# Kernel optimization log

Hardware: AMD Instinct MI355X
Metric: run time of the kernel (lower is better)

The kernel has to match this reference:

```python
import jax, jax.numpy as jnp
import numpy as np

D_MODEL = 128; D_STATE = 16; D_CONV = 4; EXPAND = 2
D_INNER = EXPAND * D_MODEL          # 256
DT_RANK = (D_MODEL + 15) // 16      # 8 (ceil(d_model/16), Mamba default)
B, NF, H, W = 4, 32, 16, 16         # L = NF*H*W = 8192 tokens


def _layer_norm(x, w, b, eps=1e-5):
    m = x.mean(-1, keepdims=True)
    v = ((x - m) ** 2).mean(-1, keepdims=True)
    return (x - m) * jax.lax.rsqrt(v + eps) * w + b


def _causal_conv(x, w, b):
    # x: [B, L, D_INNER]; w: [D_INNER, 1, D_CONV] depthwise causal conv along L
    y = jax.lax.conv_general_dilated(
        jnp.swapaxes(x, 1, 2), w, (1,), [(D_CONV - 1, 0)],
        dimension_numbers=('NCH', 'OIH', 'NCH'), feature_group_count=D_INNER)
    return jnp.swapaxes(y + b[None, :, None], 1, 2)


def _mamba_dir(xi, z, conv_w, conv_b, xproj_w, dtproj_w, dtproj_b, A_log, Dskip):
    # One direction of the bidirectional Mamba block (selective scan).
    xc = jax.nn.silu(_causal_conv(xi, conv_w, conv_b))            # [B,L,Di]
    dbl = xc @ xproj_w.T                                          # [B,L,dt_rank+2n]
    dt_r, Bm, Cm = jnp.split(dbl, [DT_RANK, DT_RANK + D_STATE], axis=-1)
    dt = jax.nn.softplus(dt_r @ dtproj_w.T + dtproj_b)            # [B,L,Di]
    A = -jnp.exp(A_log)                                           # [Di,n]

    def step(h, inp):
        dt_t, B_t, C_t, x_t = inp                                 # [B,Di],[B,n],[B,n],[B,Di]
        h = jnp.exp(dt_t[:, :, None] * A) * h + (dt_t * x_t)[:, :, None] * B_t[:, None, :]
        return h, jnp.einsum('bdn,bn->bd', h, C_t)

    h0 = jnp.zeros((xi.shape[0], D_INNER, D_STATE), xi.dtype)
    xs = tuple(jnp.swapaxes(a, 0, 1) for a in (dt, Bm, Cm, xc))   # L-leading
    _, ys = jax.lax.scan(step, h0, xs)                            # [L,B,Di]
    y = jnp.swapaxes(ys, 0, 1) + xc * Dskip
    return y * jax.nn.silu(z)


def setup_inputs() -> dict:
    key = jax.random.key(0)
    ks = jax.random.split(key, 12)
    wrand = lambda k, shape: jax.random.normal(k, shape, jnp.float32) * 0.02
    # S4D-real init: A = [1..d_state] per channel
    A_init = jnp.log(jnp.tile(jnp.arange(1, D_STATE + 1, dtype=jnp.float32)[None, :], (D_INNER, 1)))
    dt_bias = jnp.full((D_INNER,), -4.6, jnp.float32)  # softplus^-1(~0.01)
    return {
        'x': jax.random.normal(ks[0], (B, D_MODEL, NF, H, W), jnp.float32),
        'ln1_w': jnp.ones((D_MODEL,), jnp.float32), 'ln1_b': jnp.zeros((D_MODEL,), jnp.float32),
        'ln2_w': jnp.ones((D_MODEL,), jnp.float32), 'ln2_b': jnp.zeros((D_MODEL,), jnp.float32),
        'in_proj_w': wrand(ks[1], (2 * D_INNER, D_MODEL)),
        'out_proj_w': wrand(ks[2], (D_MODEL, D_INNER)),
        'conv_w_f': wrand(ks[3], (D_INNER, 1, D_CONV)), 'conv_b_f': jnp.zeros((D_INNER,), jnp.float32),
        'xproj_w_f': wrand(ks[4], (DT_RANK + 2 * D_STATE, D_INNER)),
        'dtproj_w_f': wrand(ks[5], (D_INNER, DT_RANK)), 'dtproj_b_f': dt_bias,
        'A_log_f': A_init, 'D_f': jnp.ones((D_INNER,), jnp.float32),
        'conv_w_b': wrand(ks[6], (D_INNER, 1, D_CONV)), 'conv_b_b': jnp.zeros((D_INNER,), jnp.float32),
        'xproj_w_b': wrand(ks[7], (DT_RANK + 2 * D_STATE, D_INNER)),
        'dtproj_w_b': wrand(ks[8], (D_INNER, DT_RANK)), 'dtproj_b_b': dt_bias,
        'A_log_b': A_init, 'D_b': jnp.ones((D_INNER,), jnp.float32),
    }


def reference(x, ln1_w, ln1_b, ln2_w, ln2_b, in_proj_w, out_proj_w,
              conv_w_f, conv_b_f, xproj_w_f, dtproj_w_f, dtproj_b_f, A_log_f, D_f,
              conv_w_b, conv_b_b, xproj_w_b, dtproj_w_b, dtproj_b_b, A_log_b, D_b):
    b, d, nf, h, w = x.shape
    L = nf * h * w
    x_flat = jnp.swapaxes(x.reshape(b, d, L), 1, 2)               # [B,L,d_model]
    xn = _layer_norm(x_flat, ln1_w, ln1_b)
    xz = xn @ in_proj_w.T                                          # [B,L,2*Di]
    xi, z = jnp.split(xz, 2, axis=-1)
    y_f = _mamba_dir(xi, z, conv_w_f, conv_b_f, xproj_w_f, dtproj_w_f, dtproj_b_f, A_log_f, D_f)
    y_b = _mamba_dir(xi[:, ::-1], z[:, ::-1], conv_w_b, conv_b_b, xproj_w_b,
                     dtproj_w_b, dtproj_b_b, A_log_b, D_b)[:, ::-1]
    out = (y_f + y_b) @ out_proj_w.T                               # shared out_proj
    x_out = _layer_norm(x_flat + out, ln2_w, ln2_b)                # residual + norm2
    return jnp.swapaxes(x_out, 1, 2).reshape(b, d, nf, h, w)
```

## Files before the change

kernel.cpp:

```cpp
#include <hip/hip_runtime.h>

#define NB   4
#define LSEQ 8192
#define DM   128
#define DI   256
#define NS   16
#define RK   8
#define NCH  256
#define LC   32
#define MTOT (NB*LSEQ)
#define LOG2E 1.44269504088896340736f
#define LN2f  0.69314718055994530942f

#if __has_builtin(__builtin_amdgcn_exp2f)
__device__ __forceinline__ float fexp2(float x){ return __builtin_amdgcn_exp2f(x); }
#else
__device__ __forceinline__ float fexp2(float x){ return exp2f(x); }
#endif
#if __has_builtin(__builtin_amdgcn_logf)
__device__ __forceinline__ float flog2(float x){ return __builtin_amdgcn_logf(x); }
#else
__device__ __forceinline__ float flog2(float x){ return log2f(x); }
#endif
#if __has_builtin(__builtin_amdgcn_rcpf)
__device__ __forceinline__ float frcp(float x){ return __builtin_amdgcn_rcpf(x); }
#else
__device__ __forceinline__ float frcp(float x){ return 1.f/x; }
#endif
__device__ __forceinline__ float fexpn(float x){ return fexp2(x*LOG2E); }
__device__ __forceinline__ float fsilu(float x){ return x*frcp(1.f + fexpn(-x)); }
__device__ __forceinline__ float fsoftplus(float x){
  return fmaxf(x,0.f) + flog2(1.f + fexpn(-fabsf(x)))*LN2f;
}

__device__ __forceinline__ unsigned short f2bf(float v){
  unsigned int u = __float_as_uint(v);
  return (unsigned short)((u + 0x7FFFu + ((u >> 16) & 1u)) >> 16);
}
__device__ __forceinline__ float bf2f(unsigned short h){
  return __uint_as_float(((unsigned int)h) << 16);
}

typedef __attribute__((ext_vector_type(8))) short bf16x8;
typedef __attribute__((ext_vector_type(4))) float f32x4;

__global__ __launch_bounds__(256) void k_prep_w(
    const float* __restrict__ w, unsigned short* __restrict__ hi, unsigned short* __restrict__ lo,
    const float* __restrict__ xwf, const float* __restrict__ xwb, unsigned short* __restrict__ xwbf,
    const float* __restrict__ wop, unsigned short* __restrict__ wopbf)
{
  int i = blockIdx.x*256 + threadIdx.x;
  if (i < 65536) {
    float v = w[i];
    unsigned short h = f2bf(v);
    hi[i] = h;
    lo[i] = f2bf(v - bf2f(h));
  } else if (i < 90112) {
    int j = i - 65536;
    int dirw = j / 12288;
    int rem = j - dirw*12288;
    int row = rem >> 8, k = rem & 255;
    const float* src = dirw ? xwb : xwf;
    xwbf[j] = (row < 40) ? f2bf(src[row*256 + k]) : (unsigned short)0;
  } else {
    int j = i - 90112;
    wopbf[j] = f2bf(wop[j]);
  }
}

__global__ __launch_bounds__(256) void k_ln(
    const float* __restrict__ x, const float* __restrict__ ln1w, const float* __restrict__ ln1b,
    unsigned short* __restrict__ xnh, unsigned short* __restrict__ xnl)
{
  __shared__ float a_s[DM][65];
  __shared__ float mS[64], rS[64];
  const int tid = threadIdx.x;
  const int m0 = blockIdx.x * 64;
  const int b = m0 >> 13, l0 = m0 & (LSEQ-1);
  const float* xb = x + b*DM*LSEQ;
#pragma unroll
  for (int i = 0; i < 32; ++i) {
    int idx = tid + i*256;
    int d = idx >> 6, l = idx & 63;
    a_s[d][l] = xb[d*LSEQ + l0 + l];
  }
  __syncthreads();
  {
    int p = tid & 3, l = tid >> 2;
    float s = 0.f, q = 0.f;
#pragma unroll
    for (int jj = 0; jj < 32; ++jj) {
      float v = a_s[p + 4*jj][l];
      s += v; q += v*v;
    }
    s += __shfl_xor(s,1); s += __shfl_xor(s,2);
    q += __shfl_xor(q,1); q += __shfl_xor(q,2);
    float m = s*(1.f/DM);
    float var = q*(1.f/DM) - m*m;
    if (p == 0) { mS[l] = m; rS[l] = rsqrtf(var + 1e-5f); }
  }
  __syncthreads();
#pragma unroll
  for (int i = 0; i < 32; ++i) {
    int idx = tid + i*256;
    int l = idx >> 7, d = idx & 127;
    float v = (a_s[d][l] - mS[l])*rS[l]*ln1w[d] + ln1b[d];
    unsigned short h = f2bf(v);
    xnh[(m0+l)*DM + d] = h;
    xnl[(m0+l)*DM + d] = f2bf(v - bf2f(h));
  }
}

__global__ __launch_bounds__(256) void k_gemm_in(
    const unsigned short* __restrict__ xnh, const unsigned short* __restrict__ xnl,
    const unsigned short* __restrict__ wh,  const unsigned short* __restrict__ wl,
    float* __restrict__ xi, float* __restrict__ zz)
{
  __shared__ char lds[65536];
  const int tid = threadIdx.x;
  const int m0 = blockIdx.x * 64;
  const int n0 = blockIdx.y * 64;
  const unsigned short* srcs[4] = { xnh + m0*DM, xnl + m0*DM, wh + n0*DM, wl + n0*DM };
#pragma unroll
  for (int p = 0; p < 4; ++p) {
#pragma unroll
    for (int i = 0; i < 4; ++i) {
      int u = tid + i*256;
      int row = u >> 4, c = u & 15;
      int dstu = p*1024 + row*16 + (c ^ (row & 7));
      *(uint4*)(lds + dstu*16) = *(const uint4*)(srcs[p] + row*DM + c*8);
    }
  }
  __syncthreads();
  const int wid = tid >> 6, lane = tid & 63;
  const int m0w = (wid & 1)*32, n0w = (wid >> 1)*32;
  const int lr = lane & 15, kg = lane >> 4;
  bf16x8 ah[2][4], al[2][4], bh[2][4], bl[2][4];
#pragma unroll
  for (int mi = 0; mi < 2; ++mi) {
    int row = m0w + mi*16 + lr;
#pragma unroll
    for (int kk = 0; kk < 4; ++kk) {
      int slot = (kk*4 + kg) ^ (row & 7);
      ah[mi][kk] = *(const bf16x8*)(lds + 0     + row*256 + slot*16);
      al[mi][kk] = *(const bf16x8*)(lds + 16384 + row*256 + slot*16);
    }
  }
#pragma unroll
  for (int nj = 0; nj < 2; ++nj) {
    int row = n0w + nj*16 + lr;
#pragma unroll
    for (int kk = 0; kk < 4; ++kk) {
      int slot = (kk*4 + kg) ^ (row & 7);
      bh[nj][kk] = *(const bf16x8*)(lds + 32768 + row*256 + slot*16);
      bl[nj][kk] = *(const bf16x8*)(lds + 49152 + row*256 + slot*16);
    }
  }
  f32x4 acc[2][2];
#pragma unroll
  for (int mi = 0; mi < 2; ++mi)
#pragma unroll
    for (int nj = 0; nj < 2; ++nj) acc[mi][nj] = 0.f;
#pragma unroll
  for (int kk = 0; kk < 4; ++kk)
#pragma unroll
    for (int mi = 0; mi < 2; ++mi)
#pragma unroll
      for (int nj = 0; nj < 2; ++nj)
        acc[mi][nj] = __builtin_amdgcn_mfma_f32_16x16x32_bf16(ah[mi][kk], bh[nj][kk], acc[mi][nj], 0,0,0);
#pragma unroll
  for (int kk = 0; kk < 4; ++kk)
#pragma unroll
    for (int mi = 0; mi < 2; ++mi)
#pragma unroll
      for (int nj = 0; nj < 2; ++nj)
        acc[mi][nj] = __builtin_amdgcn_mfma_f32_16x16x32_bf16(ah[mi][kk], bl[nj][kk], acc[mi][nj], 0,0,0);
#pragma unroll
  for (int kk = 0; kk < 4; ++kk)
#pragma unroll
    for (int mi = 0; mi < 2; ++mi)
#pragma unroll
      for (int nj = 0; nj < 2; ++nj)
        acc[mi][nj] = __builtin_amdgcn_mfma_f32_16x16x32_bf16(al[mi][kk], bh[nj][kk], acc[mi][nj], 0,0,0);
  float* base = (n0 < 256) ? xi : zz;
  const int ncol0 = (n0 < 256) ? n0 : n0 - 256;
#pragma unroll
  for (int mi = 0; mi < 2; ++mi)
#pragma unroll
    for (int nj = 0; nj < 2; ++nj) {
      int n_g = ncol0 + n0w + nj*16 + lr;
#pragma unroll
      for (int r = 0; r < 4; ++r) {
        int m_g = m0 + m0w + mi*16 + kg*4 + r;
        base[m_g*DI + n_g] = acc[mi][nj][r];
      }
    }
}

__global__ __launch_bounds__(256) void k_conv_xproj(
  const float* __restrict__ xi,
  const float* __restrict__ cwf, const float* __restrict__ cbf,
  const float* __restrict__ cwb, const float* __restrict__ cbb,
  const unsigned short* __restrict__ xwbf,
  float* __restrict__ dtr, float* __restrict__ Bm, float* __restrict__ Cm)
{
  __shared__ char lds[57344];
  const int tid = threadIdx.x, bid = blockIdx.x;
  const int lt = bid & (LSEQ/64 - 1);
  const int b  = (bid >> 7) & 3;
  const int dir = bid >> 9;
  const int l0 = lt*64;
  const int db = dir*NB + b;
  const unsigned short* xwp = xwbf + dir*48*256;
#pragma unroll
  for (int i = 0; i < 6; ++i) {
    int u = tid + i*256;
    int row = u >> 5, s = u & 31;
    *(uint4*)(lds + 32768 + row*512 + ((s ^ (row & 7))<<4)) =
        *(const uint4*)(xwp + row*256 + s*8);
  }
  const float* cw  = dir ? cwb : cwf;
  const float* cbp = dir ? cbb : cbf;
  const int d = tid;
  const float w0 = cw[d*4+0], w1 = cw[d*4+1], w2 = cw[d*4+2], w3 = cw[d*4+3];
  const float bias = cbp[d];
  const int g0 = dir ? (LSEQ-1-l0) : l0;
  const int stp = dir ? -DI : DI;
  const float* xp = xi + (b*LSEQ)*DI + d + g0*DI;
  float h3 = 0.f, h2 = 0.f, h1 = 0.f;
  if (l0 >= 3) { h3 = xp[-3*stp]; h2 = xp[-2*stp]; h1 = xp[-1*stp]; }
  float r0 = xp[0], r1 = xp[stp], r2 = xp[2*stp], r3 = xp[3*stp];
  for (int j = 0; j < 64; j += 4) {
    float v0 = r0, v1 = r1, v2 = r2, v3 = r3;
    if (j + 4 < 64) {
      const float* q = xp + (j+4)*stp;
      r0 = q[0]; r1 = q[stp]; r2 = q[2*stp]; r3 = q[3*stp];
    }
    float a;
#pragma unroll
    for (int u = 0; u < 4; ++u) {
      float vv = (u==0)?v0:(u==1)?v1:(u==2)?v2:v3;
      a = bias + w0*h3 + w1*h2 + w2*h1 + w3*vv;
      int row = j + u;
      *(unsigned short*)(lds + row*512 + ((((d>>3) ^ (row&7))<<4) + ((d&7)<<1))) = f2bf(fsilu(a));
      h3 = h2; h2 = h1; h1 = vv;
    }
  }
  __syncthreads();
  const int wid = tid >> 6, lane = tid & 63;
  const int lr = lane & 15, kg = lane >> 4;
  const int arow = wid*16 + lr;
  f32x4 acc[3];
#pragma unroll
  for (int j = 0; j < 3; ++j) acc[j] = 0.f;
#pragma unroll
  for (int t = 0; t < 8; ++t) {
    bf16x8 af = *(const bf16x8*)(lds + arow*512 + (((t*4+kg) ^ (arow&7))<<4));
#pragma unroll
    for (int j = 0; j < 3; ++j) {
      int wrow = j*16 + lr;
      bf16x8 bfr = *(const bf16x8*)(lds + 32768 + wrow*512 + (((t*4+kg) ^ (wrow&7))<<4));
      acc[j] = __builtin_amdgcn_mfma_f32_16x16x32_bf16(af, bfr, acc[j], 0,0,0);
    }
  }
  const int base_l = (db*LSEQ + l0) + wid*16 + kg*4;
#pragma unroll
  for (int j = 0; j < 3; ++j) {
    int col = j*16 + lr;
#pragma unroll
    for (int r = 0; r < 4; ++r) {
      int gl = base_l + r;
      float v = acc[j][r];
      if (col < 8)       dtr[gl*RK + col] = v;
      else if (col < 24) Bm[gl*NS + col - 8] = v;
      else if (col < 40) Cm[gl*NS + col - 24] = v;
    }
  }
}

__global__ __launch_bounds__(256) void k_scan_local(
  const float* __restrict__ xi, const float* __restrict__ dtr, const float* __restrict__ Bm,
  const float* __restrict__ cwf, const float* __restrict__ cbf,
  const float* __restrict__ cwb, const float* __restrict__ cbb,
  const float* __restrict__ dtwf, const float* __restrict__ dtbf,
  const float* __restrict__ dtwb, const float* __restrict__ dtbb,
  const float* __restrict__ alogf, const float* __restrict__ alogb,
  float* __restrict__ hloc, float* __restrict__ sumdt)
{
  __shared__ float Bc[LC][NS];
  __shared__ float dts[LC][RK];
  const int tid = threadIdx.x, bid = blockIdx.x;
  const int c = bid & (NCH-1), b = (bid>>8)&3, dir = bid>>10;
  const int db = dir*NB + b;
  const int l0 = c*LC;
  for (int i = tid; i < LC*NS; i += 256) (&Bc[0][0])[i]  = Bm[(db*LSEQ + l0)*NS + i];
  for (int i = tid; i < LC*RK; i += 256) (&dts[0][0])[i] = dtr[(db*LSEQ + l0)*RK + i];
  const float* cw  = dir ? cwb : cwf;
  const float* cbp = dir ? cbb : cbf;
  const float* dtw = dir ? dtwb : dtwf;
  const float* dtbp= dir ? dtbb : dtbf;
  const float* alog= dir ? alogb : alogf;
  const int d = tid;
  const float w0 = cw[d*4+0], w1 = cw[d*4+1], w2 = cw[d*4+2], w3 = cw[d*4+3];
  const float cbias = cbp[d];
  float dw[RK];
#pragma unroll
  for (int r = 0; r < RK; ++r) dw[r] = dtw[d*RK+r];
  const float dtbv = dtbp[d];
  float A2[NS];
#pragma unroll
  for (int n = 0; n < NS; ++n) A2[n] = -fexpn(alog[d*NS+n]) * LOG2E;
  const float a20 = A2[0];
  bool pw = true;
#pragma unroll
  for (int n = 1; n < NS; ++n) pw = pw && (fabsf(A2[n] - (n+1)*a20) <= 1e-3f*fabsf(A2[n]));
  float h[NS];
#pragma unroll
  for (int n = 0; n < NS; ++n) h[n] = 0.f;
  const int g0 = dir ? (LSEQ-1-l0) : l0;
  const int stp = dir ? -DI : DI;
  const float* xp = xi + (b*LSEQ)*DI + d + g0*DI;
  float h3=0.f, h2=0.f, h1=0.f;
  if (l0 >= 3) { h3 = xp[-3*stp]; h2 = xp[-2*stp]; h1 = xp[-1*stp]; }
  float r0 = xp[0], r1 = xp[stp], r2 = xp[2*stp], r3 = xp[3*stp];
  __syncthreads();
  float sac = 0.f;
  for (int j = 0; j < LC; j += 4) {
    float v0=r0, v1=r1, v2=r2, v3=r3;
    if (j + 4 < LC) { const float* q = xp + (j+4)*stp; r0=q[0]; r1=q[stp]; r2=q[2*stp]; r3=q[3*stp]; }
#pragma unroll
    for (int u = 0; u < 4; ++u) {
      float v = (u==0)?v0:(u==1)?v1:(u==2)?v2:v3;
      float a = cbias + w0*h3 + w1*h2 + w2*h1 + w3*v;
      float xc = fsilu(a);
      float dd8[RK];
      *(float4*)(dd8+0) = *(const float4*)&dts[j+u][0];
      *(float4*)(dd8+4) = *(const float4*)&dts[j+u][4];
      float sd = dtbv;
#pragma unroll
      for (int r = 0; r < RK; ++r) sd = fmaf(dw[r], dd8[r], sd);
      float dt = fsoftplus(sd);
      sac += dt;
      float dx = dt*xc;
      float bb[NS];
      *(float4*)(bb+0)  = *(const float4*)&Bc[j+u][0];
      *(float4*)(bb+4)  = *(const float4*)&Bc[j+u][4];
      *(float4*)(bb+8)  = *(const float4*)&Bc[j+u][8];
      *(float4*)(bb+12) = *(const float4*)&Bc[j+u][12];
      float earr[NS];
      if (pw) {
        float e1 = fexp2(a20*dt);
        float e = e1; earr[0] = e;
#pragma unroll
        for (int n = 1; n < NS; ++n) { e *= e1; earr[n] = e; }
      } else {
#pragma unroll
        for (int n = 0; n < NS; ++n) earr[n] = fexp2(A2[n]*dt);
      }
#pragma unroll
      for (int n = 0; n < NS; ++n) h[n] = fmaf(h[n], earr[n], dx*bb[n]);
      h3 = h2; h2 = h1; h1 = v;
    }
  }
  const int hb = ((db*NCH + c)*DI + d)*NS;
#pragma unroll
  for (int n = 0; n < NS; ++n) hloc[hb+n] = h[n];
  sumdt[(db*NCH + c)*DI + d] = sac;
}

__global__ __launch_bounds__(64) void k_prefix(
  float* __restrict__ hloc, const float* __restrict__ sumdt,
  const float* __restrict__ alogf, const float* __restrict__ alogb)
{
  const int gid = blockIdx.x*64 + threadIdx.x;
  const int n = gid & 15;
  const int d = (gid >> 4) & 255;
  const int db = gid >> 12;
  const float* alog = (db >= NB) ? alogb : alogf;
  const float a2 = -fexpn(alog[d*NS+n]) * LOG2E;
  const int HS = DI*NS;
  float* hp = hloc + (size_t)db*NCH*HS + d*NS + n;
  const float* sp = sumdt + (size_t)db*NCH*DI + d;
  float hr = 0.f;
  float bl[16], bs[16];
#pragma unroll
  for (int j = 0; j < 16; ++j) { bl[j] = hp[j*HS]; bs[j] = sp[j*DI]; }
  for (int blk = 0; blk < NCH/16; ++blk) {
    float nl[16], nsv[16];
    if (blk < NCH/16 - 1) {
#pragma unroll
      for (int j = 0; j < 16; ++j) { nl[j] = hp[(blk*16+16+j)*HS]; nsv[j] = sp[(blk*16+16+j)*DI]; }
    }
#pragma unroll
    for (int j = 0; j < 16; ++j) {
      float hl = bl[j];
      hp[(blk*16+j)*HS] = hr;
      hr = fmaf(fexp2(a2*bs[j]), hr, hl);
    }
    if (blk < NCH/16 - 1) {
#pragma unroll
      for (int j = 0; j < 16; ++j) { bl[j] = nl[j]; bs[j] = nsv[j]; }
    }
  }
}

__global__ __launch_bounds__(256) void k_scan_out(
  const float* __restrict__ xi, const float* __restrict__ zb,
  const float* __restrict__ dtr, const float* __restrict__ Bm, const float* __restrict__ Cm,
  const float* __restrict__ hin,
  const float* __restrict__ cwf, const float* __restrict__ cbf,
  const float* __restrict__ cwb, const float* __restrict__ cbb,
  const float* __restrict__ dtwf, const float* __restrict__ dtbf,
  const float* __restrict__ dtwb, const float* __restrict__ dtbb,
  const float* __restrict__ alogf, const float* __restrict__ alogb,
  const float* __restrict__ Dskf, const float* __restrict__ Dskb,
  unsigned short* __restrict__ s2bf)
{
  __shared__ float Bc[LC][NS];
  __shared__ float Cc[LC][NS];
  __shared__ float dts[LC][RK];
  const int tid = threadIdx.x, bid = blockIdx.x;
  const int c = bid & (NCH-1), b = (bid>>8)&3, dir = bid>>10;
  const int db = dir*NB + b;
  const int l0 = c*LC;
  for (int i = tid; i < LC*NS; i += 256) (&Bc[0][0])[i]  = Bm[(db*LSEQ + l0)*NS + i];
  for (int i = tid; i < LC*NS; i += 256) (&Cc[0][0])[i]  = Cm[(db*LSEQ + l0)*NS + i];
  for (int i = tid; i < LC*RK; i += 256) (&dts[0][0])[i] = dtr[(db*LSEQ + l0)*RK + i];
  const float* cw  = dir ? cwb : cwf;
  const float* cbp = dir ? cbb : cbf;
  const float* dtw = dir ? dtwb : dtwf;
  const float* dtbp= dir ? dtbb : dtbf;
  const float* alog= dir ? alogb : alogf;
  const int d = tid;
  const float w0 = cw[d*4+0], w1 = cw[d*4+1], w2 = cw[d*4+2], w3 = cw[d*4+3];
  const float cbias = cbp[d];
  const float Dd = (dir ? Dskb : Dskf)[d];
  float dw[RK];
#pragma unroll
  for (int r = 0; r < RK; ++r) dw[r] = dtw[d*RK+r];
  const float dtbv = dtbp[d];
  float A2[NS];
#pragma unroll
  for (int n = 0; n < NS; ++n) A2[n] = -fexpn(alog[d*NS+n]) * LOG2E;
  const float a20 = A2[0];
  bool pw = true;
#pragma unroll
  for (int n = 1; n < NS; ++n) pw = pw && (fabsf(A2[n] - (n+1)*a20) <= 1e-3f*fabsf(A2[n]));
  const int hb = ((db*NCH + c)*DI + d)*NS;
  float h[NS];
#pragma unroll
  for (int n = 0; n < NS; ++n) h[n] = hin[hb+n];
  const int g0 = dir ? (LSEQ-1-l0) : l0;
  const int stp = dir ? -DI : DI;
  const float* xp = xi + (b*LSEQ)*DI + d + g0*DI;
  const float* zp = zb + (b*LSEQ)*DI + d + g0*DI;
  unsigned short* sp = s2bf + (size_t)(db*LSEQ + l0)*DI + d;
  float h3=0.f, h2=0.f, h1=0.f;
  if (l0 >= 3) { h3 = xp[-3*stp]; h2 = xp[-2*stp]; h1 = xp[-1*stp]; }
  float r0 = xp[0], r1 = xp[stp], r2 = xp[2*stp], r3 = xp[3*stp];
  float z0 = zp[0], z1 = zp[stp], z2 = zp[2*stp], z3 = zp[3*stp];
  __syncthreads();
  for (int j = 0; j < LC; j += 4) {
    float v0=r0, v1=r1, v2=r2, v3=r3;
    float y0=z0, y1=z1, y2=z2, y3=z3;
    if (j + 4 < LC) {
      const float* q = xp + (j+4)*stp; r0=q[0]; r1=q[stp]; r2=q[2*stp]; r3=q[3*stp];
      const float* qz = zp + (j+4)*stp; z0=qz[0]; z1=qz[stp]; z2=qz[2*stp]; z3=qz[3*stp];
    }
#pragma unroll
    for (int u = 0; u < 4; ++u) {
      float v  = (u==0)?v0:(u==1)?v1:(u==2)?v2:v3;
      float zv = (u==0)?y0:(u==1)?y1:(u==2)?y2:y3;
      float a = cbias + w0*h3 + w1*h2 + w2*h1 + w3*v;
      float xc = fsilu(a);
      float dd8[RK];
      *(float4*)(dd8+0) = *(const float4*)&dts[j+u][0];
      *(float4*)(dd8+4) = *(const float4*)&dts[j+u][4];
      float sd = dtbv;
#pragma unroll
      for (int r = 0; r < RK; ++r) sd = fmaf(dw[r], dd8[r], sd);
      float dt = fsoftplus(sd);
      float dx = dt*xc;
      float bb[NS], ccv[NS];
      *(float4*)(bb+0)  = *(const float4*)&Bc[j+u][0];
      *(float4*)(bb+4)  = *(const float4*)&Bc[j+u][4];
      *(float4*)(bb+8)  = *(const float4*)&Bc[j+u][8];
      *(float4*)(bb+12) = *(const float4*)&Bc[j+u][12];
      *(float4*)(ccv+0)  = *(const float4*)&Cc[j+u][0];
      *(float4*)(ccv+4)  = *(const float4*)&Cc[j+u][4];
      *(float4*)(ccv+8)  = *(const float4*)&Cc[j+u][8];
      *(float4*)(ccv+12) = *(const float4*)&Cc[j+u][12];
      float earr[NS];
      if (pw) {
        float e1 = fexp2(a20*dt);
        float e = e1; earr[0] = e;
#pragma unroll
        for (int n = 1; n < NS; ++n) { e *= e1; earr[n] = e; }
      } else {
#pragma unroll
        for (int n = 0; n < NS; ++n) earr[n] = fexp2(A2[n]*dt);
      }
      float yv = 0.f;
#pragma unroll
      for (int n = 0; n < NS; ++n) {
        h[n] = fmaf(h[n], earr[n], dx*bb[n]);
        yv = fmaf(h[n], ccv[n], yv);
      }
      yv = fmaf(xc, Dd, yv);
      sp[(j+u)*DI] = f2bf(yv * fsilu(zv));
      h3 = h2; h2 = h1; h1 = v;
    }
  }
}

__global__ __launch_bounds__(512) void k_out(
  const unsigned short* __restrict__ s2bf,
  const unsigned short* __restrict__ wopbf,
  const float* __restrict__ x, const float* __restrict__ ln2w, const float* __restrict__ ln2b,
  float* __restrict__ out)
{
  __shared__ char lds[65536];
  const int tid = threadIdx.x;
  const int m0 = blockIdx.x*64;
  const int b = m0 >> 13, l0 = m0 & (LSEQ-1);
  const unsigned short* sF = s2bf + (size_t)b*LSEQ*DI;
  const unsigned short* sB = s2bf + (size_t)(NB + b)*LSEQ*DI;
#pragma unroll
  for (int i = 0; i < 8; ++i) {
    int u = tid + i*512;
    int row = u >> 6, c = u & 63;
    int l = l0 + row;
    const unsigned short* src = (c < 32) ? (sF + (size_t)l*DI + c*8)
                                         : (sB + (size_t)(LSEQ-1-l)*DI + (c-32)*8);
    *(uint4*)(lds + row*1024 + ((c ^ (row & 7))<<4)) = *(const uint4*)src;
  }
  const int wid = tid >> 6;
  const int wr = wid >> 2, wc = wid & 3;
  const int lane = tid & 63, lr = lane & 15, kg = lane >> 4;
  bf16x8 wf[2][8];
#pragma unroll
  for (int nt = 0; nt < 2; ++nt) {
    int n = wc*32 + nt*16 + lr;
#pragma unroll
    for (int kt = 0; kt < 8; ++kt)
      wf[nt][kt] = *(const bf16x8*)(wopbf + n*DI + kt*32 + kg*8);
  }
  __syncthreads();
  f32x4 acc[2][2];
#pragma unroll
  for (int mt = 0; mt < 2; ++mt)
#pragma unroll
    for (int nt = 0; nt < 2; ++nt) acc[mt][nt] = 0.f;
#pragma unroll
  for (int kt2 = 0; kt2 < 16; ++kt2) {
#pragma unroll
    for (int mt = 0; mt < 2; ++mt) {
      int row = wr*32 + mt*16 + lr;
      int slot = (kt2*4 + kg) ^ (row & 7);
      bf16x8 af = *(const bf16x8*)(lds + row*1024 + (slot<<4));
#pragma unroll
      for (int nt = 0; nt < 2; ++nt)
        acc[mt][nt] = __builtin_amdgcn_mfma_f32_16x16x32_bf16(af, wf[nt][kt2 & 7], acc[mt][nt], 0,0,0);
    }
  }
  __syncthreads();
  float* smem = (float*)lds;
  const int RP = 133;
  float* mS = smem + 64*RP;
  float* rS = mS + 64;
  const float* xb = x + b*DM*LSEQ + l0;
#pragma unroll
  for (int mt = 0; mt < 2; ++mt) {
    int mbase = wr*32 + mt*16 + kg*4;
#pragma unroll
    for (int nt = 0; nt < 2; ++nt) {
      int n = wc*32 + nt*16 + lr;
      float4 rx = *(const float4*)&xb[n*LSEQ + mbase];
      smem[(mbase+0)*RP + n] = acc[mt][nt][0] + rx.x;
      smem[(mbase+1)*RP + n] = acc[mt][nt][1] + rx.y;
      smem[(mbase+2)*RP + n] = acc[mt][nt][2] + rx.z;
      smem[(mbase+3)*RP + n] = acc[mt][nt][3] + rx.w;
    }
  }
  __syncthreads();
  {
    int row = tid >> 3, p = tid & 7;
    float s = 0.f, q = 0.f;
#pragma unroll
    for (int jj = 0; jj < 16; ++jj) {
      float v = smem[row*RP + p*16 + jj];
      s += v; q += v*v;
    }
    s += __shfl_xor(s,1); s += __shfl_xor(s,2); s += __shfl_xor(s,4);
    q += __shfl_xor(q,1); q += __shfl_xor(q,2); q += __shfl_xor(q,4);
    if (p == 0) {
      float m = s*(1.f/DM);
      float var = q*(1.f/DM) - m*m;
      mS[row] = m; rS[row] = rsqrtf(var + 1e-5f);
    }
  }
  __syncthreads();
  float* ob = out + b*DM*LSEQ + l0;
#pragma unroll
  for (int i = 0; i < 16; ++i) {
    int idx = tid + i*512;
    int col = idx >> 6, l = idx & 63;
    float v = (smem[l*RP + col] - mS[l])*rS[l]*ln2w[col] + ln2b[col];
    ob[col*LSEQ + l] = v;
  }
}

extern "C" void kernel_launch(void* const* d_in, const int* in_sizes, int n_in,
                              void* d_out, int out_size, void* d_ws, size_t ws_size,
                              hipStream_t stream)
{
  (void)in_sizes; (void)n_in; (void)out_size; (void)ws_size;
  const float* x     = (const float*)d_in[0];
  const float* ln1w  = (const float*)d_in[1];
  const float* ln1b  = (const float*)d_in[2];
  const float* ln2w  = (const float*)d_in[3];
  const float* ln2b  = (const float*)d_in[4];
  const float* wip   = (const float*)d_in[5];
  const float* wop   = (const float*)d_in[6];
  const float* cwf   = (const float*)d_in[7];
  const float* cbf   = (const float*)d_in[8];
  const float* xwf   = (const float*)d_in[9];
  const float* dtwf  = (const float*)d_in[10];
  const float* dtbf  = (const float*)d_in[11];
  const float* alogf = (const float*)d_in[12];
  const float* Dskf  = (const float*)d_in[13];
  const float* cwb   = (const float*)d_in[14];
  const float* cbb   = (const float*)d_in[15];
  const float* xwb   = (const float*)d_in[16];
  const float* dtwb  = (const float*)d_in[17];
  const float* dtbb  = (const float*)d_in[18];
  const float* alogb = (const float*)d_in[19];
  const float* Dskb  = (const float*)d_in[20];

  float* ws    = (float*)d_ws;
  float* xi    = ws;
  float* zz    = xi   + 8388608;
  float* dtr   = zz   + 8388608;
  float* Bm    = dtr  + 524288;
  float* Cm    = Bm   + 1048576;
  float* s2    = Cm   + 1048576;
  float* hloc  = s2   + 16777216;
  float* sumdt = hloc + 8388608;
  float* xwbfF = sumdt + 524288;
  float* wopbfF= xwbfF + 12288;
  float* out   = (float*)d_out;
  unsigned short* xnh = (unsigned short*)s2;
  unsigned short* xnl = (unsigned short*)(s2 + 2097152);
  unsigned short* whp = (unsigned short*)(s2 + 4194304);
  unsigned short* wlp = (unsigned short*)(s2 + 4227072);
  unsigned short* s2bf = (unsigned short*)s2;
  unsigned short* xwbf = (unsigned short*)xwbfF;
  unsigned short* wopbf = (unsigned short*)wopbfF;

  k_prep_w<<<480, 256, 0, stream>>>(wip, whp, wlp, xwf, xwb, xwbf, wop, wopbf);
  k_ln<<<512, 256, 0, stream>>>(x, ln1w, ln1b, xnh, xnl);
  k_gemm_in<<<dim3(512,8), 256, 0, stream>>>(xnh, xnl, whp, wlp, xi, zz);
  k_conv_xproj<<<1024, 256, 0, stream>>>(xi, cwf,cbf,cwb,cbb, xwbf, dtr, Bm, Cm);
  k_scan_local<<<2048, 256, 0, stream>>>(xi, dtr, Bm, cwf,cbf,cwb,cbb,
                                         dtwf,dtbf,dtwb,dtbb, alogf, alogb, hloc, sumdt);
  k_prefix<<<512, 64, 0, stream>>>(hloc, sumdt, alogf, alogb);
  k_scan_out<<<2048, 256, 0, stream>>>(xi, zz, dtr, Bm, Cm, hloc, cwf,cbf,cwb,cbb,
                                       dtwf,dtbf,dtwb,dtbb, alogf,alogb, Dskf, Dskb, s2bf);
  k_out<<<512, 512, 0, stream>>>(s2bf, wopbf, x, ln2w, ln2b, out);
}
```

Measured before the change: 186.9 us.

## Drop split-bf16 in-proj, precompute conv/dt once, store bf16 intermediates

The input projection now uses a single bf16 MFMA pass instead of the three-pass hi/lo split, and z is stored as bf16. The conv+silu output and the softplus dt are computed once in k_conv_xproj and packed as a bf16 pair per element. Both scan kernels then read this packed buffer instead of each recomputing the conv and dt projection from fp32 xi. Chunk states in hloc are also stored as bf16. This cuts memory traffic and redundant arithmetic at the cost of lower precision in dt, xc, z and the carried scan state.

```diff
diff --git a/kernel.cpp b/kernel.cpp
--- a/kernel.cpp
+++ b/kernel.cpp
@@ -45,16 +45,13 @@
 typedef __attribute__((ext_vector_type(4))) float f32x4;
 
 __global__ __launch_bounds__(256) void k_prep_w(
-    const float* __restrict__ w, unsigned short* __restrict__ hi, unsigned short* __restrict__ lo,
+    const float* __restrict__ wip, unsigned short* __restrict__ wipbf,
     const float* __restrict__ xwf, const float* __restrict__ xwb, unsigned short* __restrict__ xwbf,
     const float* __restrict__ wop, unsigned short* __restrict__ wopbf)
 {
   int i = blockIdx.x*256 + threadIdx.x;
   if (i < 65536) {
-    float v = w[i];
-    unsigned short h = f2bf(v);
-    hi[i] = h;
-    lo[i] = f2bf(v - bf2f(h));
+    wipbf[i] = f2bf(wip[i]);
   } else if (i < 90112) {
     int j = i - 65536;
     int dirw = j / 12288;
@@ -70,7 +67,7 @@
 
 __global__ __launch_bounds__(256) void k_ln(
     const float* __restrict__ x, const float* __restrict__ ln1w, const float* __restrict__ ln1b,
-    unsigned short* __restrict__ xnh, unsigned short* __restrict__ xnl)
+    unsigned short* __restrict__ xnbf)
 {
   __shared__ float a_s[DM][65];
   __shared__ float mS[64], rS[64];
@@ -105,24 +102,21 @@
     int idx = tid + i*256;
     int l = idx >> 7, d = idx & 127;
     float v = (a_s[d][l] - mS[l])*rS[l]*ln1w[d] + ln1b[d];
-    unsigned short h = f2bf(v);
-    xnh[(m0+l)*DM + d] = h;
-    xnl[(m0+l)*DM + d] = f2bf(v - bf2f(h));
+    xnbf[(m0+l)*DM + d] = f2bf(v);
   }
 }
 
 __global__ __launch_bounds__(256) void k_gemm_in(
-    const unsigned short* __restrict__ xnh, const unsigned short* __restrict__ xnl,
-    const unsigned short* __restrict__ wh,  const unsigned short* __restrict__ wl,
-    float* __restrict__ xi, float* __restrict__ zz)
-{
-  __shared__ char lds[65536];
+    const unsigned short* __restrict__ xnbf, const unsigned short* __restrict__ wipbf,
+    float* __restrict__ xi, unsigned short* __restrict__ zzb)
+{
+  __shared__ char lds[32768];
   const int tid = threadIdx.x;
   const int m0 = blockIdx.x * 64;
   const int n0 = blockIdx.y * 64;
-  const unsigned short* srcs[4] = { xnh + m0*DM, xnl + m0*DM, wh + n0*DM, wl + n0*DM };
-#pragma unroll
-  for (int p = 0; p < 4; ++p) {
+  const unsigned short* srcs[2] = { xnbf + m0*DM, wipbf + n0*DM };
+#pragma unroll
+  for (int p = 0; p < 2; ++p) {
 #pragma unroll
     for (int i = 0; i < 4; ++i) {
       int u = tid + i*256;
@@ -135,15 +129,14 @@
   const int wid = tid >> 6, lane = tid & 63;
   const int m0w = (wid & 1)*32, n0w = (wid >> 1)*32;
   const int lr = lane & 15, kg = lane >> 4;
-  bf16x8 ah[2][4], al[2][4], bh[2][4], bl[2][4];
+  bf16x8 af[2][4], bfv[2][4];
 #pragma unroll
   for (int mi = 0; mi < 2; ++mi) {
     int row = m0w + mi*16 + lr;
 #pragma unroll
     for (int kk = 0; kk < 4; ++kk) {
       int slot = (kk*4 + kg) ^ (row & 7);
-      ah[mi][kk] = *(const bf16x8*)(lds + 0     + row*256 + slot*16);
-      al[mi][kk] = *(const bf16x8*)(lds + 16384 + row*256 + slot*16);
+      af[mi][kk] = *(const bf16x8*)(lds + row*256 + slot*16);
     }
   }
 #pragma unroll
@@ -152,8 +145,7 @@
 #pragma unroll
     for (int kk = 0; kk < 4; ++kk) {
       int slot = (kk*4 + kg) ^ (row & 7);
-      bh[nj][kk] = *(const bf16x8*)(lds + 32768 + row*256 + slot*16);
-      bl[nj][kk] = *(const bf16x8*)(lds + 49152 + row*256 + slot*16);
+      bfv[nj][kk] = *(const bf16x8*)(lds + 16384 + row*256 + slot*16);
     }
   }
   f32x4 acc[2][2];
@@ -167,34 +159,32 @@
     for (int mi = 0; mi < 2; ++mi)
 #pragma unroll
       for (int nj = 0; nj < 2; ++nj)
-        acc[mi][nj] = __builtin_amdgcn_mfma_f32_16x16x32_bf16(ah[mi][kk], bh[nj][kk], acc[mi][nj], 0,0,0);
-#pragma unroll
-  for (int kk = 0; kk < 4; ++kk)
+        acc[mi][nj] = __builtin_amdgcn_mfma_f32_16x16x32_bf16(af[mi][kk], bfv[nj][kk], acc[mi][nj], 0,0,0);
+  if (n0 < 256) {
 #pragma unroll
     for (int mi = 0; mi < 2; ++mi)
 #pragma unroll
-      for (int nj = 0; nj < 2; ++nj)
-        acc[mi][nj] = __builtin_amdgcn_mfma_f32_16x16x32_bf16(ah[mi][kk], bl[nj][kk], acc[mi][nj], 0,0,0);
-#pragma unroll
-  for (int kk = 0; kk < 4; ++kk)
+      for (int nj = 0; nj < 2; ++nj) {
+        int n_g = n0 + n0w + nj*16 + lr;
+#pragma unroll
+        for (int r = 0; r < 4; ++r) {
+          int m_g = m0 + m0w + mi*16 + kg*4 + r;
+          xi[(size_t)m_g*DI + n_g] = acc[mi][nj][r];
+        }
+      }
+  } else {
 #pragma unroll
     for (int mi = 0; mi < 2; ++mi)
 #pragma unroll
-      for (int nj = 0; nj < 2; ++nj)
-        acc[mi][nj] = __builtin_amdgcn_mfma_f32_16x16x32_bf16(al[mi][kk], bh[nj][kk], acc[mi][nj], 0,0,0);
-  float* base = (n0 < 256) ? xi : zz;
-  const int ncol0 = (n0 < 256) ? n0 : n0 - 256;
-#pragma unroll
-  for (int mi = 0; mi < 2; ++mi)
-#pragma unroll
-    for (int nj = 0; nj < 2; ++nj) {
-      int n_g = ncol0 + n0w + nj*16 + lr;
-#pragma unroll
-      for (int r = 0; r < 4; ++r) {
-        int m_g = m0 + m0w + mi*16 + kg*4 + r;
-        base[m_g*DI + n_g] = acc[mi][nj][r];
+      for (int nj = 0; nj < 2; ++nj) {
+        int n_g = (n0 - 256) + n0w + nj*16 + lr;
+#pragma unroll
+        for (int r = 0; r < 4; ++r) {
+          int m_g = m0 + m0w + mi*16 + kg*4 + r;
+          zzb[(size_t)m_g*DI + n_g] = f2bf(acc[mi][nj][r]);
+        }
       }
-    }
+  }
 }
 
 __global__ __launch_bounds__(256) void k_conv_xproj(
@@ -202,9 +192,13 @@
   const float* __restrict__ cwf, const float* __restrict__ cbf,
   const float* __restrict__ cwb, const float* __restrict__ cbb,
   const unsigned short* __restrict__ xwbf,
-  float* __restrict__ dtr, float* __restrict__ Bm, float* __restrict__ Cm)
+  const float* __restrict__ dtwf, const float* __restrict__ dtbf,
+  const float* __restrict__ dtwb, const float* __restrict__ dtbb,
+  float* __restrict__ Bm, float* __restrict__ Cm,
+  unsigned int* __restrict__ xdt)
 {
   __shared__ char lds[57344];
+  __shared__ float dtr_s[64][8];
   const int tid = threadIdx.x, bid = blockIdx.x;
   const int lt = bid & (LSEQ/64 - 1);
   const int b  = (bid >> 7) & 3;
@@ -226,7 +220,9 @@
   const float bias = cbp[d];
   const int g0 = dir ? (LSEQ-1-l0) : l0;
   const int stp = dir ? -DI : DI;
-  const float* xp = xi + (b*LSEQ)*DI + d + g0*DI;
+  const float* xp = xi + (size_t)(b*LSEQ)*DI + d + (size_t)g0*DI;
+  unsigned short* xdt_us = (unsigned short*)xdt;
+  const size_t obase = ((size_t)(db*LSEQ + l0))*DI + d;
   float h3 = 0.f, h2 = 0.f, h1 = 0.f;
   if (l0 >= 3) { h3 = xp[-3*stp]; h2 = xp[-2*stp]; h1 = xp[-1*stp]; }
   float r0 = xp[0], r1 = xp[stp], r2 = xp[2*stp], r3 = xp[3*stp];
@@ -236,13 +232,14 @@
       const float* q = xp + (j+4)*stp;
       r0 = q[0]; r1 = q[stp]; r2 = q[2*stp]; r3 = q[3*stp];
     }
-    float a;
 #pragma unroll
     for (int u = 0; u < 4; ++u) {
       float vv = (u==0)?v0:(u==1)?v1:(u==2)?v2:v3;
-      a = bias + w0*h3 + w1*h2 + w2*h1 + w3*vv;
+      float a = bias + w0*h3 + w1*h2 + w2*h1 + w3*vv;
       int row = j + u;
-      *(unsigned short*)(lds + row*512 + ((((d>>3) ^ (row&7))<<4) + ((d&7)<<1))) = f2bf(fsilu(a));
+      unsigned short xcb = f2bf(fsilu(a));
+      *(unsigned short*)(lds + row*512 + ((((d>>3) ^ (row&7))<<4) + ((d&7)<<1))) = xcb;
+      xdt_us[(obase + (size_t)row*DI)*2] = xcb;
       h3 = h2; h2 = h1; h1 = vv;
     }
   }
@@ -255,58 +252,55 @@
   for (int j = 0; j < 3; ++j) acc[j] = 0.f;
 #pragma unroll
   for (int t = 0; t < 8; ++t) {
-    bf16x8 af = *(const bf16x8*)(lds + arow*512 + (((t*4+kg) ^ (arow&7))<<4));
+    bf16x8 afv = *(const bf16x8*)(lds + arow*512 + (((t*4+kg) ^ (arow&7))<<4));
 #pragma unroll
     for (int j = 0; j < 3; ++j) {
       int wrow = j*16 + lr;
       bf16x8 bfr = *(const bf16x8*)(lds + 32768 + wrow*512 + (((t*4+kg) ^ (wrow&7))<<4));
-      acc[j] = __builtin_amdgcn_mfma_f32_16x16x32_bf16(af, bfr, acc[j], 0,0,0);
+      acc[j] = __builtin_amdgcn_mfma_f32_16x16x32_bf16(afv, bfr, acc[j], 0,0,0);
     }
   }
   const int base_l = (db*LSEQ + l0) + wid*16 + kg*4;
+  const int rloc = wid*16 + kg*4;
 #pragma unroll
   for (int j = 0; j < 3; ++j) {
     int col = j*16 + lr;
 #pragma unroll
     for (int r = 0; r < 4; ++r) {
-      int gl = base_l + r;
       float v = acc[j][r];
-      if (col < 8)       dtr[gl*RK + col] = v;
-      else if (col < 24) Bm[gl*NS + col - 8] = v;
-      else if (col < 40) Cm[gl*NS + col - 24] = v;
-    }
+      if (col < 8)       dtr_s[rloc + r][col] = v;
+      else if (col < 24) Bm[(size_t)(base_l + r)*NS + col - 8] = v;
+      else if (col < 40) Cm[(size_t)(base_l + r)*NS + col - 24] = v;
+    }
+  }
+  __syncthreads();
+  const float* dtw = dir ? dtwb : dtwf;
+  const float* dtbp= dir ? dtbb : dtbf;
+  float dwv[8];
+  *(float4*)(dwv+0) = *(const float4*)&dtw[d*RK];
+  *(float4*)(dwv+4) = *(const float4*)&dtw[d*RK+4];
+  const float dtbv = dtbp[d];
+  for (int row = 0; row < 64; ++row) {
+    float sd = dtbv;
+#pragma unroll
+    for (int r = 0; r < RK; ++r) sd = fmaf(dtr_s[row][r], dwv[r], sd);
+    xdt_us[(obase + (size_t)row*DI)*2 + 1] = f2bf(fsoftplus(sd));
   }
 }
 
 __global__ __launch_bounds__(256) void k_scan_local(
-  const float* __restrict__ xi, const float* __restrict__ dtr, const float* __restrict__ Bm,
-  const float* __restrict__ cwf, const float* __restrict__ cbf,
-  const float* __restrict__ cwb, const float* __restrict__ cbb,
-  const float* __restrict__ dtwf, const float* __restrict__ dtbf,
-  const float* __restrict__ dtwb, const float* __restrict__ dtbb,
+  const unsigned int* __restrict__ xdt, const float* __restrict__ Bm,
   const float* __restrict__ alogf, const float* __restrict__ alogb,
-  float* __restrict__ hloc, float* __restrict__ sumdt)
+  unsigned short* __restrict__ hloc, float* __restrict__ sumdt)
 {
   __shared__ float Bc[LC][NS];
-  __shared__ float dts[LC][RK];
   const int tid = threadIdx.x, bid = blockIdx.x;
   const int c = bid & (NCH-1), b = (bid>>8)&3, dir = bid>>10;
   const int db = dir*NB + b;
   const int l0 = c*LC;
-  for (int i = tid; i < LC*NS; i += 256) (&Bc[0][0])[i]  = Bm[(db*LSEQ + l0)*NS + i];
-  for (int i = tid; i < LC*RK; i += 256) (&dts[0][0])[i] = dtr[(db*LSEQ + l0)*RK + i];
-  const float* cw  = dir ? cwb : cwf;
-  const float* cbp = dir ? cbb : cbf;
-  const float* dtw = dir ? dtwb : dtwf;
-  const float* dtbp= dir ? dtbb : dtbf;
-  const float* alog= dir ? alogb : alogf;
+  for (int i = tid; i < LC*NS; i += 256) (&Bc[0][0])[i] = Bm[(size_t)(db*LSEQ + l0)*NS + i];
+  const float* alog = dir ? alogb : alogf;
   const int d = tid;
-  const float w0 = cw[d*4+0], w1 = cw[d*4+1], w2 = cw[d*4+2], w3 = cw[d*4+3];
-  const float cbias = cbp[d];
-  float dw[RK];
-#pragma unroll
-  for (int r = 0; r < RK; ++r) dw[r] = dtw[d*RK+r];
-  const float dtbv = dtbp[d];
   float A2[NS];
 #pragma unroll
   for (int n = 0; n < NS; ++n) A2[n] = -fexpn(alog[d*NS+n]) * LOG2E;
@@ -317,29 +311,21 @@
   float h[NS];
 #pragma unroll
   for (int n = 0; n < NS; ++n) h[n] = 0.f;
-  const int g0 = dir ? (LSEQ-1-l0) : l0;
-  const int stp = dir ? -DI : DI;
-  const float* xp = xi + (b*LSEQ)*DI + d + g0*DI;
-  float h3=0.f, h2=0.f, h1=0.f;
-  if (l0 >= 3) { h3 = xp[-3*stp]; h2 = xp[-2*stp]; h1 = xp[-1*stp]; }
-  float r0 = xp[0], r1 = xp[stp], r2 = xp[2*stp], r3 = xp[3*stp];
+  const unsigned int* xp = xdt + (size_t)(db*LSEQ + l0)*DI + d;
+  unsigned int u0 = xp[0], u1 = xp[DI], u2 = xp[2*DI], u3 = xp[3*DI];
   __syncthreads();
   float sac = 0.f;
   for (int j = 0; j < LC; j += 4) {
-    float v0=r0, v1=r1, v2=r2, v3=r3;
-    if (j + 4 < LC) { const float* q = xp + (j+4)*stp; r0=q[0]; r1=q[stp]; r2=q[2*stp]; r3=q[3*stp]; }
+    unsigned int w0=u0, w1=u1, w2=u2, w3=u3;
+    if (j + 4 < LC) {
+      const unsigned int* q = xp + (size_t)(j+4)*DI;
+      u0=q[0]; u1=q[DI]; u2=q[2*DI]; u3=q[3*DI];
+    }
 #pragma unroll
     for (int u = 0; u < 4; ++u) {
-      float v = (u==0)?v0:(u==1)?v1:(u==2)?v2:v3;
-      float a = cbias + w0*h3 + w1*h2 + w2*h1 + w3*v;
-      float xc = fsilu(a);
-      float dd8[RK];
-      *(float4*)(dd8+0) = *(const float4*)&dts[j+u][0];
-      *(float4*)(dd8+4) = *(const float4*)&dts[j+u][4];
-      float sd = dtbv;
-#pragma unroll
-      for (int r = 0; r < RK; ++r) sd = fmaf(dw[r], dd8[r], sd);
-      float dt = fsoftplus(sd);
+      unsigned int uu = (u==0)?w0:(u==1)?w1:(u==2)?w2:w3;
+      float xc = __uint_as_float(uu << 16);
+      float dt = __uint_as_float(uu & 0xffff0000u);
       sac += dt;
       float dx = dt*xc;
       float bb[NS];
@@ -359,17 +345,20 @@
       }
 #pragma unroll
       for (int n = 0; n < NS; ++n) h[n] = fmaf(h[n], earr[n], dx*bb[n]);
-      h3 = h2; h2 = h1; h1 = v;
-    }
-  }
-  const int hb = ((db*NCH + c)*DI + d)*NS;
-#pragma unroll
-  for (int n = 0; n < NS; ++n) hloc[hb+n] = h[n];
-  sumdt[(db*NCH + c)*DI + d] = sac;
+    }
+  }
+  unsigned int hp8[8];
+#pragma unroll
+  for (int k = 0; k < 8; ++k)
+    hp8[k] = (unsigned int)f2bf(h[2*k]) | ((unsigned int)f2bf(h[2*k+1]) << 16);
+  unsigned short* dst = hloc + ((size_t)(db*NCH + c)*DI + d)*NS;
+  *(uint4*)(dst)   = *(uint4*)(hp8);
+  *(uint4*)(dst+8) = *(uint4*)(hp8+4);
+  sumdt[(size_t)(db*NCH + c)*DI + d] = sac;
 }
 
 __global__ __launch_bounds__(64) void k_prefix(
-  float* __restrict__ hloc, const float* __restrict__ sumdt,
+  unsigned short* __restrict__ hloc, const float* __restrict__ sumdt,
   const float* __restrict__ alogf, const float* __restrict__ alogb)
 {
   const int gid = blockIdx.x*64 + threadIdx.x;
@@ -379,22 +368,25 @@
   const float* alog = (db >= NB) ? alogb : alogf;
   const float a2 = -fexpn(alog[d*NS+n]) * LOG2E;
   const int HS = DI*NS;
-  float* hp = hloc + (size_t)db*NCH*HS + d*NS + n;
+  unsigned short* hp = hloc + (size_t)db*NCH*HS + d*NS + n;
   const float* sp = sumdt + (size_t)db*NCH*DI + d;
   float hr = 0.f;
   float bl[16], bs[16];
 #pragma unroll
-  for (int j = 0; j < 16; ++j) { bl[j] = hp[j*HS]; bs[j] = sp[j*DI]; }
+  for (int j = 0; j < 16; ++j) { bl[j] = bf2f(hp[(size_t)j*HS]); bs[j] = sp[(size_t)j*DI]; }
   for (int blk = 0; blk < NCH/16; ++blk) {
     float nl[16], nsv[16];
     if (blk < NCH/16 - 1) {
 #pragma unroll
-      for (int j = 0; j < 16; ++j) { nl[j] = hp[(blk*16+16+j)*HS]; nsv[j] = sp[(blk*16+16+j)*DI]; }
+      for (int j = 0; j < 16; ++j) {
+        nl[j]  = bf2f(hp[(size_t)(blk*16+16+j)*HS]);
+        nsv[j] = sp[(size_t)(blk*16+16+j)*DI];
+      }
     }
 #pragma unroll
     for (int j = 0; j < 16; ++j) {
       float hl = bl[j];
-      hp[(blk*16+j)*HS] = hr;
+      hp[(size_t)(blk*16+j)*HS] = f2bf(hr);
       hr = fmaf(fexp2(a2*bs[j]), hr, hl);
     }
     if (blk < NCH/16 - 1) {
@@ -405,40 +397,24 @@
 }
 
 __global__ __launch_bounds__(256) void k_scan_out(
-  const float* __restrict__ xi, const float* __restrict__ zb,
-  const float* __restrict__ dtr, const float* __restrict__ Bm, const float* __restrict__ Cm,
-  const float* __restrict__ hin,
-  const float* __restrict__ cwf, const float* __restrict__ cbf,
-  const float* __restrict__ cwb, const float* __restrict__ cbb,
-  const float* __restrict__ dtwf, const float* __restrict__ dtbf,
-  const float* __restrict__ dtwb, const float* __restrict__ dtbb,
+  const unsigned int* __restrict__ xdt, const unsigned short* __restrict__ zzb,
+  const float* __restrict__ Bm, const float* __restrict__ Cm,
+  const unsigned short* __restrict__ hinb,
   const float* __restrict__ alogf, const float* __restrict__ alogb,
   const float* __restrict__ Dskf, const float* __restrict__ Dskb,
   unsigned short* __restrict__ s2bf)
 {
   __shared__ float Bc[LC][NS];
   __shared__ float Cc[LC][NS];
-  __shared__ float dts[LC][RK];
   const int tid = threadIdx.x, bid = blockIdx.x;
   const int c = bid & (NCH-1), b = (bid>>8)&3, dir = bid>>10;
   const int db = dir*NB + b;
   const int l0 = c*LC;
-  for (int i = tid; i < LC*NS; i += 256) (&Bc[0][0])[i]  = Bm[(db*LSEQ + l0)*NS + i];
-  for (int i = tid; i < LC*NS; i += 256) (&Cc[0][0])[i]  = Cm[(db*LSEQ + l0)*NS + i];
-  for (int i = tid; i < LC*RK; i += 256) (&dts[0][0])[i] = dtr[(db*LSEQ + l0)*RK + i];
-  const float* cw  = dir ? cwb : cwf;
-  const float* cbp = dir ? cbb : cbf;
-  const float* dtw = dir ? dtwb : dtwf;
-  const float* dtbp= dir ? dtbb : dtbf;
-  const float* alog= dir ? alogb : alogf;
+  for (int i = tid; i < LC*NS; i += 256) (&Bc[0][0])[i] = Bm[(size_t)(db*LSEQ + l0)*NS + i];
+  for (int i = tid; i < LC*NS; i += 256) (&Cc[0][0])[i] = Cm[(size_t)(db*LSEQ + l0)*NS + i];
+  const float* alog = dir ? alogb : alogf;
   const int d = tid;
-  const float w0 = cw[d*4+0], w1 = cw[d*4+1], w2 = cw[d*4+2], w3 = cw[d*4+3];
-  const float cbias = cbp[d];
   const float Dd = (dir ? Dskb : Dskf)[d];
-  float dw[RK];
-#pragma unroll
-  for (int r = 0; r < RK; ++r) dw[r] = dtw[d*RK+r];
-  const float dtbv = dtbp[d];
   float A2[NS];
 #pragma unroll
   for (int n = 0; n < NS; ++n) A2[n] = -fexpn(alog[d*NS+n]) * LOG2E;
@@ -446,40 +422,41 @@
   bool pw = true;
 #pragma unroll
   for (int n = 1; n < NS; ++n) pw = pw && (fabsf(A2[n] - (n+1)*a20) <= 1e-3f*fabsf(A2[n]));
-  const int hb = ((db*NCH + c)*DI + d)*NS;
   float h[NS];
-#pragma unroll
-  for (int n = 0; n < NS; ++n) h[n] = hin[hb+n];
+  {
+    const unsigned short* hb = hinb + ((size_t)(db*NCH + c)*DI + d)*NS;
+    uint4 p0 = *(const uint4*)(hb);
+    uint4 p1 = *(const uint4*)(hb+8);
+    unsigned int w[8] = {p0.x,p0.y,p0.z,p0.w,p1.x,p1.y,p1.z,p1.w};
+#pragma unroll
+    for (int k = 0; k < 8; ++k) {
+      h[2*k]   = __uint_as_float(w[k] << 16);
+      h[2*k+1] = __uint_as_float(w[k] & 0xffff0000u);
+    }
+  }
   const int g0 = dir ? (LSEQ-1-l0) : l0;
   const int stp = dir ? -DI : DI;
-  const float* xp = xi + (b*LSEQ)*DI + d + g0*DI;
-  const float* zp = zb + (b*LSEQ)*DI + d + g0*DI;
+  const unsigned int* xp = xdt + (size_t)(db*LSEQ + l0)*DI + d;
+  const unsigned short* zp = zzb + (size_t)(b*LSEQ + g0)*DI + d;
   unsigned short* sp = s2bf + (size_t)(db*LSEQ + l0)*DI + d;
-  float h3=0.f, h2=0.f, h1=0.f;
-  if (l0 >= 3) { h3 = xp[-3*stp]; h2 = xp[-2*stp]; h1 = xp[-1*stp]; }
-  float r0 = xp[0], r1 = xp[stp], r2 = xp[2*stp], r3 = xp[3*stp];
-  float z0 = zp[0], z1 = zp[stp], z2 = zp[2*stp], z3 = zp[3*stp];
+  unsigned int u0 = xp[0], u1 = xp[DI], u2 = xp[2*DI], u3 = xp[3*DI];
+  unsigned short z0 = zp[0], z1 = zp[stp], z2 = zp[2*stp], z3 = zp[3*stp];
   __syncthreads();
   for (int j = 0; j < LC; j += 4) {
-    float v0=r0, v1=r1, v2=r2, v3=r3;
-    float y0=z0, y1=z1, y2=z2, y3=z3;
+    unsigned int w0=u0, w1=u1, w2=u2, w3=u3;
+    unsigned short y0=z0, y1=z1, y2=z2, y3=z3;
     if (j + 4 < LC) {
-      const float* q = xp + (j+4)*stp; r0=q[0]; r1=q[stp]; r2=q[2*stp]; r3=q[3*stp];
-      const float* qz = zp + (j+4)*stp; z0=qz[0]; z1=qz[stp]; z2=qz[2*stp]; z3=qz[3*stp];
+      const unsigned int* q = xp + (size_t)(j+4)*DI;
+      u0=q[0]; u1=q[DI]; u2=q[2*DI]; u3=q[3*DI];
+      const unsigned short* qz = zp + (j+4)*stp;
+      z0=qz[0]; z1=qz[stp]; z2=qz[2*stp]; z3=qz[3*stp];
     }
 #pragma unroll
     for (int u = 0; u < 4; ++u) {
-      float v  = (u==0)?v0:(u==1)?v1:(u==2)?v2:v3;
-      float zv = (u==0)?y0:(u==1)?y1:(u==2)?y2:y3;
-      float a = cbias + w0*h3 + w1*h2 + w2*h1 + w3*v;
-      float xc = fsilu(a);
-      float dd8[RK];
-      *(float4*)(dd8+0) = *(const float4*)&dts[j+u][0];
-      *(float4*)(dd8+4) = *(const float4*)&dts[j+u][4];
-      float sd = dtbv;
-#pragma unroll
-      for (int r = 0; r < RK; ++r) sd = fmaf(dw[r], dd8[r], sd);
-      float dt = fsoftplus(sd);
+      unsigned int uu = (u==0)?w0:(u==1)?w1:(u==2)?w2:w3;
+      unsigned short zu = (u==0)?y0:(u==1)?y1:(u==2)?y2:y3;
+      float xc = __uint_as_float(uu << 16);
+      float dt = __uint_as_float(uu & 0xffff0000u);
       float dx = dt*xc;
       float bb[NS], ccv[NS];
       *(float4*)(bb+0)  = *(const float4*)&Bc[j+u][0];
@@ -507,8 +484,8 @@
         yv = fmaf(h[n], ccv[n], yv);
       }
       yv = fmaf(xc, Dd, yv);
-      sp[(j+u)*DI] = f2bf(yv * fsilu(zv));
-      h3 = h2; h2 = h1; h1 = v;
+      float zv = bf2f(zu);
+      sp[(size_t)(j+u)*DI] = f2bf(yv * fsilu(zv));
     }
   }
 }
@@ -639,32 +616,33 @@
 
   float* ws    = (float*)d_ws;
   float* xi    = ws;
-  float* zz    = xi   + 8388608;
-  float* dtr   = zz   + 8388608;
-  float* Bm    = dtr  + 524288;
-  float* Cm    = Bm   + 1048576;
-  float* s2    = Cm   + 1048576;
-  float* hloc  = s2   + 16777216;
-  float* sumdt = hloc + 8388608;
+  float* zzbF  = xi    + 8388608;
+  float* Bm    = zzbF  + 4194304;
+  float* Cm    = Bm    + 1048576;
+  float* s2F   = Cm    + 1048576;
+  float* xdtF  = s2F   + 8388608;
+  float* hlocF = xdtF  + 16777216;
+  float* sumdt = hlocF + 4194304;
   float* xwbfF = sumdt + 524288;
   float* wopbfF= xwbfF + 12288;
   float* out   = (float*)d_out;
-  unsigned short* xnh = (unsigned short*)s2;
-  unsigned short* xnl = (unsigned short*)(s2 + 2097152);
-  unsigned short* whp = (unsigned short*)(s2 + 4194304);
-  unsigned short* wlp = (unsigned short*)(s2 + 4227072);
-  unsigned short* s2bf = (unsigned short*)s2;
-  unsigned short* xwbf = (unsigned short*)xwbfF;
+  unsigned short* xnbf  = (unsigned short*)s2F;
+  unsigned short* wipbf = (unsigned short*)(s2F + 2097152);
+  unsigned short* s2bf  = (unsigned short*)s2F;
+  unsigned short* zzb   = (unsigned short*)zzbF;
+  unsigned int*   xdt   = (unsigned int*)xdtF;
+  unsigned short* hloc  = (unsigned short*)hlocF;
+  unsigned short* xwbf  = (unsigned short*)xwbfF;
   unsigned short* wopbf = (unsigned short*)wopbfF;
 
-  k_prep_w<<<480, 256, 0, stream>>>(wip, whp, wlp, xwf, xwb, xwbf, wop, wopbf);
-  k_ln<<<512, 256, 0, stream>>>(x, ln1w, ln1b, xnh, xnl);
-  k_gemm_in<<<dim3(512,8), 256, 0, stream>>>(xnh, xnl, whp, wlp, xi, zz);
-  k_conv_xproj<<<1024, 256, 0, stream>>>(xi, cwf,cbf,cwb,cbb, xwbf, dtr, Bm, Cm);
-  k_scan_local<<<2048, 256, 0, stream>>>(xi, dtr, Bm, cwf,cbf,cwb,cbb,
-                                         dtwf,dtbf,dtwb,dtbb, alogf, alogb, hloc, sumdt);
+  k_prep_w<<<480, 256, 0, stream>>>(wip, wipbf, xwf, xwb, xwbf, wop, wopbf);
+  k_ln<<<512, 256, 0, stream>>>(x, ln1w, ln1b, xnbf);
+  k_gemm_in<<<dim3(512,8), 256, 0, stream>>>(xnbf, wipbf, xi, zzb);
+  k_conv_xproj<<<1024, 256, 0, stream>>>(xi, cwf,cbf,cwb,cbb, xwbf,
+                                         dtwf,dtbf,dtwb,dtbb, Bm, Cm, xdt);
+  k_scan_local<<<2048, 256, 0, stream>>>(xdt, Bm, alogf, alogb, hloc, sumdt);
   k_prefix<<<512, 64, 0, stream>>>(hloc, sumdt, alogf, alogb);
-  k_scan_out<<<2048, 256, 0, stream>>>(xi, zz, dtr, Bm, Cm, hloc, cwf,cbf,cwb,cbb,
-                                       dtwf,dtbf,dtwb,dtbb, alogf,alogb, Dskf, Dskb, s2bf);
+  k_scan_out<<<2048, 256, 0, stream>>>(xdt, zzb, Bm, Cm, hloc,
+                                       alogf, alogb, Dskf, Dskb, s2bf);
   k_out<<<512, 512, 0, stream>>>(s2bf, wopbf, x, ln2w, ln2b, out);
 }
```

New measurement: 184.2 us. About the same (-1.4%).
